# Kernel tuning notes

Measured on AMD Instinct MI355X. Metric: run time of the kernel, lower is better.

## Reference

```python
import jax, jax.numpy as jnp
import numpy as np

B, T, C, H = 2, 2048, 1024, 16
D = C // H  # head dim


def setup_inputs() -> dict:
    key = jax.random.key(0)
    k1, k2, k3 = jax.random.split(key, 3)
    x = jax.random.normal(k1, (B, T, C), dtype=jnp.float32)
    w_qkv = jax.random.normal(k2, (3 * C, C), dtype=jnp.float32) * (1.0 / np.sqrt(C))
    b_qkv = jnp.zeros((3 * C,), dtype=jnp.float32)
    w_proj = jax.random.normal(k3, (C, C), dtype=jnp.float32) * (1.0 / np.sqrt(C))
    b_proj = jnp.zeros((C,), dtype=jnp.float32)
    return {"x": x, "w_qkv": w_qkv, "b_qkv": b_qkv, "w_proj": w_proj, "b_proj": b_proj}


def reference(x, w_qkv, b_qkv, w_proj, b_proj):
    # torch Linear: y = x @ W^T + b
    qkv = jnp.einsum('btc,oc->bto', x, w_qkv) + b_qkv  # [B,T,3C]
    q, k, v = jnp.split(qkv, 3, axis=-1)
    # [B,T,C] -> [B,H,T,D]
    reshape = lambda t: t.reshape(B, T, H, D).transpose(0, 2, 1, 3)
    q, k, v = reshape(q), reshape(k), reshape(v)
    scale = 1.0 / jnp.sqrt(jnp.float32(C))  # NOTE: full C, as in source
    att = jnp.einsum('bhtd,bhsd->bhts', q, k) * scale  # [B,H,T,T]
    causal = jnp.tril(jnp.ones((T, T), dtype=bool))
    att = jnp.where(causal, att, -jnp.inf)
    att = jax.nn.softmax(att, axis=-1)
    y = jnp.einsum('bhts,bhsd->bhtd', att, v)  # [B,H,T,D]
    y = y.transpose(0, 2, 1, 3).reshape(B, T, C)
    return jnp.einsum('btc,oc->bto', y, w_proj) + b_proj
```

## Files before the change

kernel.cpp:

```cpp
#include <hip/hip_runtime.h>

#define DEVINL __device__ __forceinline__

typedef __attribute__((ext_vector_type(8))) short short8;
typedef __attribute__((ext_vector_type(4))) float f32x4;

DEVINL unsigned f2bf_u(float x) {
  union { float f; unsigned u; } v; v.f = x;
  unsigned r = v.u + 0x7FFF + ((v.u >> 16) & 1);
  return r >> 16;
}
DEVINL unsigned short f2bf(float x) { return (unsigned short)f2bf_u(x); }

DEVINL unsigned cvt_pk_bf16(float lo, float hi) {
  unsigned r;
  asm("v_cvt_pk_bf16_f32 %0, %1, %2" : "=v"(r) : "v"(lo), "v"(hi));
  return r;
}

DEVINL void permlane32_swap(unsigned& a, unsigned& b) {
  asm volatile("v_permlane32_swap_b32 %0, %1" : "+v"(a), "+v"(b));
}
DEVINL void permlane16_swap(unsigned& a, unsigned& b) {
  asm volatile("v_permlane16_swap_b32 %0, %1" : "+v"(a), "+v"(b));
}

#if __has_builtin(__builtin_amdgcn_exp2f)
#define EXP2(x) __builtin_amdgcn_exp2f(x)
#else
#define EXP2(x) exp2f(x)
#endif

DEVINL void gload_lds16(const void* g, void* l) {
  __builtin_amdgcn_global_load_lds(
      (const __attribute__((address_space(1))) unsigned int*)g,
      (__attribute__((address_space(3))) unsigned int*)l, 16, 0, 0);
}

DEVINL short8 as_s8(uint4 v) { union { uint4 u; short8 s; } c; c.u = v; return c.s; }
DEVINL f32x4 fzero() { f32x4 z = {0.f, 0.f, 0.f, 0.f}; return z; }

__global__ __launch_bounds__(256) void cvt3_kernel(
    const float4* __restrict__ x, const float4* __restrict__ wq,
    const float4* __restrict__ wp, ushort4* __restrict__ xo,
    ushort4* __restrict__ wqo, ushort4* __restrict__ wpo) {
  const int N1 = 1048576, N2 = 1835008, NT = 2097152;
  int i = blockIdx.x * blockDim.x + threadIdx.x;
  int stride = gridDim.x * blockDim.x;
  for (; i < NT; i += stride) {
    const float4* s; ushort4* d; int j;
    if (i < N1) { s = x; d = xo; j = i; }
    else if (i < N2) { s = wq; d = wqo; j = i - N1; }
    else { s = wp; d = wpo; j = i - N2; }
    float4 v = s[j];
    ushort4 o;
    o.x = f2bf(v.x); o.y = f2bf(v.y); o.z = f2bf(v.z); o.w = f2bf(v.w);
    d[j] = o;
  }
}

template <int MODE, int RX, int RY>
__global__ __launch_bounds__(256, 2) void gemm_bt(
    const ushort* __restrict__ A, const ushort* __restrict__ Bw,
    const float* __restrict__ bias,
    ushort* __restrict__ Qb, ushort* __restrict__ Kb, ushort* __restrict__ Vt,
    float* __restrict__ Out, int M, int N, int K) {
  __shared__ __align__(16) char smem[32768];
  char* ldsA = smem;
  char* ldsB = smem + 16384;

  int gx = gridDim.x;
  int id = blockIdx.y * gx + blockIdx.x;
  int xcd = id & 7, slot = id >> 3;
  int rw = gx / RX, rh = gridDim.y / RY;
  int bx = (xcd % RX) * rw + slot % rw;
  int by = (xcd / RX) * rh + slot / rw;

  int m0 = by * 128, n0 = bx * 128;
  int t = threadIdx.x;
  int lane = t & 63, w = t >> 6;
  int q = lane & 15, g = lane >> 4;
  int wr = w >> 1, wc = w & 1;

  int Lrow[4], Lcol[4];
#pragma unroll
  for (int i = 0; i < 4; ++i) {
    int L = i * 4096 + t * 16;
    int row = L >> 7, c = L & 127;
    Lrow[i] = row;
    Lcol[i] = c ^ ((row & 7) << 4);
  }
  const char* Abase = (const char*)A + (size_t)m0 * K * 2;
  const char* Bbase = (const char*)Bw + (size_t)n0 * K * 2;

  f32x4 acc[4][4];
#pragma unroll
  for (int i = 0; i < 4; ++i)
#pragma unroll
    for (int j = 0; j < 4; ++j) acc[i][j] = fzero();

  for (int k0 = 0; k0 < K; k0 += 64) {
    __syncthreads();
#pragma unroll
    for (int i = 0; i < 4; ++i) {
      int L = i * 4096 + t * 16;
      gload_lds16(Abase + (size_t)Lrow[i] * (K * 2) + k0 * 2 + Lcol[i], ldsA + L);
    }
#pragma unroll
    for (int i = 0; i < 4; ++i) {
      int L = i * 4096 + t * 16;
      gload_lds16(Bbase + (size_t)Lrow[i] * (K * 2) + k0 * 2 + Lcol[i], ldsB + L);
    }
    __syncthreads();

    uint4 bf[2][4];
#pragma unroll
    for (int s = 0; s < 2; ++s)
#pragma unroll
      for (int nt = 0; nt < 4; ++nt) {
        int row = wc * 64 + nt * 16 + q;
        int addr = row * 128 + ((g * 16 + 64 * s) ^ ((row & 7) << 4));
        bf[s][nt] = *(const uint4*)(ldsB + addr);
      }
#pragma unroll
    for (int mt = 0; mt < 4; ++mt) {
      int row = wr * 64 + mt * 16 + q;
      int a0 = row * 128 + ((g * 16) ^ ((row & 7) << 4));
      int a1 = row * 128 + ((g * 16 + 64) ^ ((row & 7) << 4));
      uint4 af0 = *(const uint4*)(ldsA + a0);
      uint4 af1 = *(const uint4*)(ldsA + a1);
#pragma unroll
      for (int nt = 0; nt < 4; ++nt) {
        acc[mt][nt] = __builtin_amdgcn_mfma_f32_16x16x32_bf16(
            as_s8(af0), as_s8(bf[0][nt]), acc[mt][nt], 0, 0, 0);
        acc[mt][nt] = __builtin_amdgcn_mfma_f32_16x16x32_bf16(
            as_s8(af1), as_s8(bf[1][nt]), acc[mt][nt], 0, 0, 0);
      }
    }
  }

  if (MODE == 0) {
    int mrow0 = m0 + wr * 64;
    int b = mrow0 >> 11, tt0 = mrow0 & 2047;
    if (n0 >= 2048) {
      int hs = (n0 + wc * 64) >> 6;
      int h = hs & 15;
      ushort* vb = Vt + ((size_t)(b * 16 + h) * 64) * 2048;
#pragma unroll
      for (int nt = 0; nt < 4; ++nt) {
        int d = nt * 16 + q;
        float bv = bias[n0 + wc * 64 + nt * 16 + q];
#pragma unroll
        for (int mt = 0; mt < 4; ++mt) {
          uint2 o;
          o.x = cvt_pk_bf16(acc[mt][nt][0] + bv, acc[mt][nt][1] + bv);
          o.y = cvt_pk_bf16(acc[mt][nt][2] + bv, acc[mt][nt][3] + bv);
          *(uint2*)(vb + (size_t)d * 2048 + tt0 + mt * 16 + g * 4) = o;
        }
      }
    } else {
      __syncthreads();
      char* tile = smem + w * 8192;
      float bv[4];
#pragma unroll
      for (int nt = 0; nt < 4; ++nt) bv[nt] = bias[n0 + wc * 64 + nt * 16 + q];
#pragma unroll
      for (int mt = 0; mt < 4; ++mt)
#pragma unroll
        for (int nt = 0; nt < 4; ++nt)
#pragma unroll
          for (int r = 0; r < 4; ++r) {
            int row = mt * 16 + g * 4 + r;
            int bcol = ((nt * 16 + q) * 2) ^ ((row & 7) << 4);
            *(ushort*)(tile + row * 128 + bcol) = f2bf(acc[mt][nt][r] + bv[nt]);
          }
      int hs = (n0 + wc * 64) >> 6;
      int which = hs >> 4, h = hs & 15;
      ushort* dst = which == 0 ? Qb : Kb;
      ushort* dbase = dst + (size_t)(b * 16 + h) * 131072 + (size_t)tt0 * 64;
#pragma unroll
      for (int p = 0; p < 8; ++p) {
        int row = p * 8 + (lane >> 3);
        int bcol = ((lane & 7) * 16) ^ ((row & 7) << 4);
        uint4 v = *(const uint4*)(tile + row * 128 + bcol);
        *(uint4*)(dbase + (size_t)row * 64 + (lane & 7) * 8) = v;
      }
    }
  } else {
#pragma unroll
    for (int nt = 0; nt < 4; ++nt) {
      int ncol = n0 + wc * 64 + nt * 16 + q;
      float bv = bias[ncol];
#pragma unroll
      for (int mt = 0; mt < 4; ++mt)
#pragma unroll
        for (int r = 0; r < 4; ++r) {
          int m = m0 + wr * 64 + mt * 16 + g * 4 + r;
          Out[(size_t)m * N + ncol] = acc[mt][nt][r] + bv;
        }
    }
  }
}

__global__ __launch_bounds__(512, 1) void attn_kernel(
    const ushort* __restrict__ Q, const ushort* __restrict__ K,
    const ushort* __restrict__ Vt, ushort* __restrict__ Y) {
  __shared__ __align__(16) char smem[65536];
  const float C44 = 0.0450842298f;
  const float THR44 = 11.5415603f;
  int id = blockIdx.x;
  int xcd = id & 7, slot = id >> 3;
  int bh = xcd * 4 + (slot >> 4);
  int pidx = slot & 15;
  int t = threadIdx.x;
  int lane = t & 63, w = t >> 6;
  int q = lane & 15, g = lane >> 4;
  int wq = w & 3, half = w >> 2;
  int b = bh >> 4, hh = bh & 15;

  const char* Kc0 = (const char*)(K + (size_t)bh * 2048 * 64);
  const char* Vc0 = (const char*)(Vt + (size_t)bh * 64 * 2048);

  int krow[2], kcol[2], vrow[2], vcol[2];
#pragma unroll
  for (int i = 0; i < 2; ++i) {
    int L = i * 8192 + t * 16;
    krow[i] = L >> 7;
    kcol[i] = (L & 127) ^ ((krow[i] & 7) << 4);
    vrow[i] = L >> 8;
    vcol[i] = (L & 255) ^ ((vrow[i] & 7) << 4);
  }
  int offK[4][2], offV[4];
#pragma unroll
  for (int sub = 0; sub < 4; ++sub)
#pragma unroll
    for (int s = 0; s < 2; ++s) {
      int row = half * 64 + sub * 16 + q;
      offK[sub][s] = row * 128 + ((g * 16 + 64 * s) ^ ((row & 7) << 4));
    }
#pragma unroll
  for (int ds = 0; ds < 4; ++ds) {
    int row = ds * 16 + q;
    offV[ds] = 16384 + row * 256 + ((half * 128 + g * 16) ^ ((row & 7) << 4));
  }
  int offV2[4];
#pragma unroll
  for (int ds = 0; ds < 4; ++ds) {
    int row = ds * 16 + q;
    offV2[ds] = 16384 + row * 256 + ((half * 128 + 64 + g * 16) ^ ((row & 7) << 4));
  }

#pragma unroll 1
  for (int pass = 0; pass < 2; ++pass) {
    int qt = pass ? pidx : 31 - pidx;
    int nch = (qt >> 1) + 1;
    int qrow0 = qt * 64 + wq * 16;
    int qg = qrow0 + q;

    uint4 qf[2];
    {
      const ushort* Qrow = Q + ((size_t)bh * 2048 + qrow0 + q) * 64;
      qf[0] = *(const uint4*)(Qrow + g * 8);
      qf[1] = *(const uint4*)(Qrow + 32 + g * 8);
    }

    f32x4 oacc[4];
#pragma unroll
    for (int i = 0; i < 4; ++i) oacc[i] = fzero();
    float m_run = -1e30f;
    float l_run = 0.f;

#pragma unroll
    for (int i = 0; i < 2; ++i) {
      int L = i * 8192 + t * 16;
      gload_lds16(Kc0 + (size_t)krow[i] * 128 + kcol[i], smem + L);
      gload_lds16(Vc0 + (size_t)vrow[i] * 4096 + vcol[i], smem + 16384 + L);
    }
    __syncthreads();

    int cur = 0;
#pragma unroll 1
    for (int c = 0; c < nch; ++c) {
      int kv0 = c * 128;
      if (c + 1 < nch) {
        int kn = kv0 + 128;
        char* dstb = smem + (cur ^ 1) * 32768;
#pragma unroll
        for (int i = 0; i < 2; ++i) {
          int L = i * 8192 + t * 16;
          gload_lds16(Kc0 + (size_t)(kn + krow[i]) * 128 + kcol[i], dstb + L);
          gload_lds16(Vc0 + (size_t)vrow[i] * 4096 + (size_t)kn * 2 + vcol[i],
                      dstb + 16384 + L);
        }
      }
      const char* base = smem + cur * 32768;
      int kst = kv0 + half * 64;
      if (kst <= qrow0 + 15) {
        f32x4 sacc[4];
        __builtin_amdgcn_s_setprio(1);
#pragma unroll
        for (int sub = 0; sub < 4; ++sub) {
          sacc[sub] = fzero();
#pragma unroll
          for (int s = 0; s < 2; ++s)
            sacc[sub] = __builtin_amdgcn_mfma_f32_16x16x32_bf16(
                as_s8(*(const uint4*)(base + offK[sub][s])), as_s8(qf[s]),
                sacc[sub], 0, 0, 0);
        }
        __builtin_amdgcn_s_setprio(0);

        float sr[4][4];
        if (kst + 63 > qrow0) {
#pragma unroll
          for (int sub = 0; sub < 4; ++sub)
#pragma unroll
            for (int r = 0; r < 4; ++r) {
              int kv = kst + sub * 16 + g * 4 + r;
              sr[sub][r] = (kv > qg) ? -3e38f : sacc[sub][r];
            }
        } else {
#pragma unroll
          for (int sub = 0; sub < 4; ++sub)
#pragma unroll
            for (int r = 0; r < 4; ++r) sr[sub][r] = sacc[sub][r];
        }
        float ms[4];
#pragma unroll
        for (int sub = 0; sub < 4; ++sub)
          ms[sub] = fmaxf(fmaxf(sr[sub][0], sr[sub][1]),
                          fmaxf(sr[sub][2], sr[sub][3]));
        float mx44 = fmaxf(fmaxf(ms[0], ms[1]), fmaxf(ms[2], ms[3])) * C44;

        if (!__all(mx44 <= m_run + THR44)) {
          mx44 = fmaxf(mx44, __shfl_xor(mx44, 16));
          mx44 = fmaxf(mx44, __shfl_xor(mx44, 32));
          float mnew = fmaxf(m_run, mx44);
          float corr = EXP2(m_run - mnew);
          float cr[4];
#pragma unroll
          for (int r = 0; r < 4; ++r) cr[r] = __shfl(corr, g * 4 + r);
#pragma unroll
          for (int ds = 0; ds < 4; ++ds)
#pragma unroll
            for (int r = 0; r < 4; ++r) oacc[ds][r] *= cr[r];
          l_run *= corr;
          m_run = mnew;
        }

        float nm = -m_run;
        unsigned pk[4][2];
        float psum = 0.f;
#pragma unroll
        for (int sub = 0; sub < 4; ++sub) {
          float p0 = EXP2(__builtin_fmaf(sr[sub][0], C44, nm));
          float p1 = EXP2(__builtin_fmaf(sr[sub][1], C44, nm));
          float p2 = EXP2(__builtin_fmaf(sr[sub][2], C44, nm));
          float p3 = EXP2(__builtin_fmaf(sr[sub][3], C44, nm));
          psum += (p0 + p1) + (p2 + p3);
          pk[sub][0] = cvt_pk_bf16(p0, p1);
          pk[sub][1] = cvt_pk_bf16(p2, p3);
        }
        l_run += psum;

        uint4 pa[2];
#pragma unroll
        for (int h = 0; h < 2; ++h) {
          unsigned w0 = pk[2 * h][0], w1 = pk[2 * h + 1][0];
          permlane32_swap(w0, w1);
          permlane16_swap(w0, w1);
          unsigned w2 = pk[2 * h][1], w3 = pk[2 * h + 1][1];
          permlane32_swap(w2, w3);
          permlane16_swap(w2, w3);
          pa[h].x = w0; pa[h].y = w2; pa[h].z = w1; pa[h].w = w3;
        }

        __builtin_amdgcn_s_setprio(1);
#pragma unroll
        for (int ds = 0; ds < 4; ++ds) {
          oacc[ds] = __builtin_amdgcn_mfma_f32_16x16x32_bf16(
              as_s8(pa[0]), as_s8(*(const uint4*)(base + offV[ds])),
              oacc[ds], 0, 0, 0);
          oacc[ds] = __builtin_amdgcn_mfma_f32_16x16x32_bf16(
              as_s8(pa[1]), as_s8(*(const uint4*)(base + offV2[ds])),
              oacc[ds], 0, 0, 0);
        }
        __builtin_amdgcn_s_setprio(0);
      }

      __syncthreads();
      cur ^= 1;
    }

    l_run += __shfl_xor(l_run, 16);
    l_run += __shfl_xor(l_run, 32);
    float* ob = (float*)smem + wq * 1024;
    float* mlb = (float*)(smem + 16384);
    if (half) {
#pragma unroll
      for (int ds = 0; ds < 4; ++ds)
#pragma unroll
        for (int r = 0; r < 4; ++r)
          ob[(g * 4 + r) * 64 + ds * 16 + q] = oacc[ds][r];
      if (g == 0) {
        mlb[wq * 32 + q] = m_run;
        mlb[wq * 32 + 16 + q] = l_run;
      }
    }
    __syncthreads();
    if (!half) {
#pragma unroll
      for (int r = 0; r < 4; ++r) {
        int row = g * 4 + r;
        float mA = __shfl(m_run, row);
        float lA = __shfl(l_run, row);
        float mB = mlb[wq * 32 + row];
        float lB = mlb[wq * 32 + 16 + row];
        float mS = fmaxf(mA, mB);
        float sA = EXP2(mA - mS), sB = EXP2(mB - mS);
        float linv = 1.0f / (lA * sA + lB * sB);
        sA *= linv; sB *= linv;
#pragma unroll
        for (int ds = 0; ds < 4; ++ds) {
          float vB = ob[row * 64 + ds * 16 + q];
          float yv = oacc[ds][r] * sA + vB * sB;
          Y[(size_t)(b * 2048 + qrow0 + row) * 1024 + hh * 64 + ds * 16 + q] =
              f2bf(yv);
        }
      }
    }
    __syncthreads();
  }
}

extern "C" void kernel_launch(void* const* d_in, const int* in_sizes, int n_in,
                              void* d_out, int out_size, void* d_ws, size_t ws_size,
                              hipStream_t stream) {
  const float* x = (const float*)d_in[0];
  const float* w_qkv = (const float*)d_in[1];
  const float* b_qkv = (const float*)d_in[2];
  const float* w_proj = (const float*)d_in[3];
  const float* b_proj = (const float*)d_in[4];
  float* out = (float*)d_out;
  char* ws = (char*)d_ws;
  const size_t MB = 1024 * 1024;
  ushort* xb    = (ushort*)(ws + 0 * MB);
  ushort* wqkvb = (ushort*)(ws + 8 * MB);
  ushort* wprojb= (ushort*)(ws + 14 * MB);
  ushort* Qb    = (ushort*)(ws + 16 * MB);
  ushort* Kb    = (ushort*)(ws + 24 * MB);
  ushort* Vt    = (ushort*)(ws + 40 * MB);
  ushort* Yb    = (ushort*)(ws + 48 * MB);

  cvt3_kernel<<<2048, 256, 0, stream>>>((const float4*)x, (const float4*)w_qkv,
                                        (const float4*)w_proj, (ushort4*)xb,
                                        (ushort4*)wqkvb, (ushort4*)wprojb);
  gemm_bt<0, 2, 4><<<dim3(24, 32), 256, 0, stream>>>(xb, wqkvb, b_qkv, Qb, Kb, Vt,
                                                     nullptr, 4096, 3072, 1024);
  attn_kernel<<<dim3(512), 512, 0, stream>>>(Qb, Kb, Vt, Yb);
  gemm_bt<1, 1, 8><<<dim3(8, 32), 256, 0, stream>>>(Yb, wprojb, b_proj, nullptr,
                                                    nullptr, nullptr, out, 4096,
                                                    1024, 1024);
}
```

Measured before the change: 95.29 us.

## Load attention K/V directly into registers and split projection GEMM into smaller tiles

The attention kernel drops its double-buffered LDS staging of K and V and has each wave load its K/V fragments straight from global memory into registers. Shared memory shrinks, per-chunk __syncthreads go away, and occupancy is raised to 4 blocks. The projection GEMM becomes a separate kernel with 64x128 tiles and a 512-block grid to fill more CUs. The cost is duplicated global/L2 reads of K/V across waves, with no prefetch to overlap load latency.

```diff
diff --git a/kernel.cpp b/kernel.cpp
--- a/kernel.cpp
+++ b/kernel.cpp
@@ -59,12 +59,12 @@
   }
 }
 
-template <int MODE, int RX, int RY>
-__global__ __launch_bounds__(256, 2) void gemm_bt(
+template <int RX, int RY>
+__global__ __launch_bounds__(256, 2) void gemm_qkv(
     const ushort* __restrict__ A, const ushort* __restrict__ Bw,
     const float* __restrict__ bias,
     ushort* __restrict__ Qb, ushort* __restrict__ Kb, ushort* __restrict__ Vt,
-    float* __restrict__ Out, int M, int N, int K) {
+    int M, int N, int K) {
   __shared__ __align__(16) char smem[32768];
   char* ldsA = smem;
   char* ldsB = smem + 16384;
@@ -139,73 +139,150 @@
     }
   }
 
-  if (MODE == 0) {
-    int mrow0 = m0 + wr * 64;
-    int b = mrow0 >> 11, tt0 = mrow0 & 2047;
-    if (n0 >= 2048) {
-      int hs = (n0 + wc * 64) >> 6;
-      int h = hs & 15;
-      ushort* vb = Vt + ((size_t)(b * 16 + h) * 64) * 2048;
+  int mrow0 = m0 + wr * 64;
+  int b = mrow0 >> 11, tt0 = mrow0 & 2047;
+  if (n0 >= 2048) {
+    int hs = (n0 + wc * 64) >> 6;
+    int h = hs & 15;
+    ushort* vb = Vt + ((size_t)(b * 16 + h) * 64) * 2048;
+#pragma unroll
+    for (int nt = 0; nt < 4; ++nt) {
+      int d = nt * 16 + q;
+      float bv = bias[n0 + wc * 64 + nt * 16 + q];
+#pragma unroll
+      for (int mt = 0; mt < 4; ++mt) {
+        uint2 o;
+        o.x = cvt_pk_bf16(acc[mt][nt][0] + bv, acc[mt][nt][1] + bv);
+        o.y = cvt_pk_bf16(acc[mt][nt][2] + bv, acc[mt][nt][3] + bv);
+        *(uint2*)(vb + (size_t)d * 2048 + tt0 + mt * 16 + g * 4) = o;
+      }
+    }
+  } else {
+    __syncthreads();
+    char* tile = smem + w * 8192;
+    float bv[4];
+#pragma unroll
+    for (int nt = 0; nt < 4; ++nt) bv[nt] = bias[n0 + wc * 64 + nt * 16 + q];
+#pragma unroll
+    for (int mt = 0; mt < 4; ++mt)
+#pragma unroll
+      for (int nt = 0; nt < 4; ++nt)
+#pragma unroll
+        for (int r = 0; r < 4; ++r) {
+          int row = mt * 16 + g * 4 + r;
+          int bcol = ((nt * 16 + q) * 2) ^ ((row & 7) << 4);
+          *(ushort*)(tile + row * 128 + bcol) = f2bf(acc[mt][nt][r] + bv[nt]);
+        }
+    int hs = (n0 + wc * 64) >> 6;
+    int which = hs >> 4, h = hs & 15;
+    ushort* dst = which == 0 ? Qb : Kb;
+    ushort* dbase = dst + (size_t)(b * 16 + h) * 131072 + (size_t)tt0 * 64;
+#pragma unroll
+    for (int p = 0; p < 8; ++p) {
+      int row = p * 8 + (lane >> 3);
+      int bcol = ((lane & 7) * 16) ^ ((row & 7) << 4);
+      uint4 v = *(const uint4*)(tile + row * 128 + bcol);
+      *(uint4*)(dbase + (size_t)row * 64 + (lane & 7) * 8) = v;
+    }
+  }
+}
+
+__global__ __launch_bounds__(256, 2) void gemm_proj(
+    const ushort* __restrict__ A, const ushort* __restrict__ Bw,
+    const float* __restrict__ bias, float* __restrict__ Out,
+    int M, int N, int K) {
+  __shared__ __align__(16) char smem[24576];
+
+  int gx = gridDim.x;
+  int id = blockIdx.y * gx + blockIdx.x;
+  int xcd = id & 7, slot = id >> 3;
+  int bx = slot & 7;
+  int by = xcd * 8 + (slot >> 3);
+
+  int m0 = by * 64, n0 = bx * 128;
+  int t = threadIdx.x;
+  int lane = t & 63, w = t >> 6;
+  int q = lane & 15, g = lane >> 4;
+  int wr = w >> 1, wc = w & 1;
+
+  int Lrow[4], Lcol[4];
+#pragma unroll
+  for (int i = 0; i < 4; ++i) {
+    int L = i * 4096 + t * 16;
+    int row = L >> 7, c = L & 127;
+    Lrow[i] = row;
+    Lcol[i] = c ^ ((row & 7) << 4);
+  }
+  const char* Abase = (const char*)A + (size_t)m0 * K * 2;
+  const char* Bbase = (const char*)Bw + (size_t)n0 * K * 2;
+
+  f32x4 acc[2][4];
+#pragma unroll
+  for (int i = 0; i < 2; ++i)
+#pragma unroll
+    for (int j = 0; j < 4; ++j) acc[i][j] = fzero();
+
+  for (int k0 = 0; k0 < K; k0 += 64) {
+    __syncthreads();
+#pragma unroll
+    for (int i = 0; i < 2; ++i) {
+      int L = i * 4096 + t * 16;
+      gload_lds16(Abase + (size_t)Lrow[i] * (K * 2) + k0 * 2 + Lcol[i], smem + L);
+    }
+#pragma unroll
+    for (int i = 0; i < 4; ++i) {
+      int L = i * 4096 + t * 16;
+      gload_lds16(Bbase + (size_t)Lrow[i] * (K * 2) + k0 * 2 + Lcol[i],
+                  smem + 8192 + L);
+    }
+    __syncthreads();
+
+    uint4 bf[2][4];
+#pragma unroll
+    for (int s = 0; s < 2; ++s)
 #pragma unroll
       for (int nt = 0; nt < 4; ++nt) {
-        int d = nt * 16 + q;
-        float bv = bias[n0 + wc * 64 + nt * 16 + q];
-#pragma unroll
-        for (int mt = 0; mt < 4; ++mt) {
-          uint2 o;
-          o.x = cvt_pk_bf16(acc[mt][nt][0] + bv, acc[mt][nt][1] + bv);
-          o.y = cvt_pk_bf16(acc[mt][nt][2] + bv, acc[mt][nt][3] + bv);
-          *(uint2*)(vb + (size_t)d * 2048 + tt0 + mt * 16 + g * 4) = o;
-        }
-      }
-    } else {
-      __syncthreads();
-      char* tile = smem + w * 8192;
-      float bv[4];
-#pragma unroll
-      for (int nt = 0; nt < 4; ++nt) bv[nt] = bias[n0 + wc * 64 + nt * 16 + q];
-#pragma unroll
-      for (int mt = 0; mt < 4; ++mt)
-#pragma unroll
-        for (int nt = 0; nt < 4; ++nt)
-#pragma unroll
-          for (int r = 0; r < 4; ++r) {
-            int row = mt * 16 + g * 4 + r;
-            int bcol = ((nt * 16 + q) * 2) ^ ((row & 7) << 4);
-            *(ushort*)(tile + row * 128 + bcol) = f2bf(acc[mt][nt][r] + bv[nt]);
-          }
-      int hs = (n0 + wc * 64) >> 6;
-      int which = hs >> 4, h = hs & 15;
-      ushort* dst = which == 0 ? Qb : Kb;
-      ushort* dbase = dst + (size_t)(b * 16 + h) * 131072 + (size_t)tt0 * 64;
-#pragma unroll
-      for (int p = 0; p < 8; ++p) {
-        int row = p * 8 + (lane >> 3);
-        int bcol = ((lane & 7) * 16) ^ ((row & 7) << 4);
-        uint4 v = *(const uint4*)(tile + row * 128 + bcol);
-        *(uint4*)(dbase + (size_t)row * 64 + (lane & 7) * 8) = v;
-      }
-    }
-  } else {
-#pragma unroll
-    for (int nt = 0; nt < 4; ++nt) {
-      int ncol = n0 + wc * 64 + nt * 16 + q;
-      float bv = bias[ncol];
-#pragma unroll
-      for (int mt = 0; mt < 4; ++mt)
-#pragma unroll
-        for (int r = 0; r < 4; ++r) {
-          int m = m0 + wr * 64 + mt * 16 + g * 4 + r;
-          Out[(size_t)m * N + ncol] = acc[mt][nt][r] + bv;
-        }
-    }
-  }
-}
-
-__global__ __launch_bounds__(512, 1) void attn_kernel(
+        int row = wc * 64 + nt * 16 + q;
+        int addr = 8192 + row * 128 + ((g * 16 + 64 * s) ^ ((row & 7) << 4));
+        bf[s][nt] = *(const uint4*)(smem + addr);
+      }
+    __builtin_amdgcn_s_setprio(1);
+#pragma unroll
+    for (int mt = 0; mt < 2; ++mt) {
+      int row = wr * 32 + mt * 16 + q;
+      int a0 = row * 128 + ((g * 16) ^ ((row & 7) << 4));
+      int a1 = row * 128 + ((g * 16 + 64) ^ ((row & 7) << 4));
+      uint4 af0 = *(const uint4*)(smem + a0);
+      uint4 af1 = *(const uint4*)(smem + a1);
+#pragma unroll
+      for (int nt = 0; nt < 4; ++nt) {
+        acc[mt][nt] = __builtin_amdgcn_mfma_f32_16x16x32_bf16(
+            as_s8(af0), as_s8(bf[0][nt]), acc[mt][nt], 0, 0, 0);
+        acc[mt][nt] = __builtin_amdgcn_mfma_f32_16x16x32_bf16(
+            as_s8(af1), as_s8(bf[1][nt]), acc[mt][nt], 0, 0, 0);
+      }
+    }
+    __builtin_amdgcn_s_setprio(0);
+  }
+
+#pragma unroll
+  for (int nt = 0; nt < 4; ++nt) {
+    int ncol = n0 + wc * 64 + nt * 16 + q;
+    float bv = bias[ncol];
+#pragma unroll
+    for (int mt = 0; mt < 2; ++mt)
+#pragma unroll
+      for (int r = 0; r < 4; ++r) {
+        int m = m0 + wr * 32 + mt * 16 + g * 4 + r;
+        Out[(size_t)m * N + ncol] = acc[mt][nt][r] + bv;
+      }
+  }
+}
+
+__global__ __launch_bounds__(512, 4) void attn_kernel(
     const ushort* __restrict__ Q, const ushort* __restrict__ K,
     const ushort* __restrict__ Vt, ushort* __restrict__ Y) {
-  __shared__ __align__(16) char smem[65536];
+  __shared__ __align__(16) char smem[20480];
   const float C44 = 0.0450842298f;
   const float THR44 = 11.5415603f;
   int id = blockIdx.x;
@@ -218,37 +295,10 @@
   int wq = w & 3, half = w >> 2;
   int b = bh >> 4, hh = bh & 15;
 
-  const char* Kc0 = (const char*)(K + (size_t)bh * 2048 * 64);
-  const char* Vc0 = (const char*)(Vt + (size_t)bh * 64 * 2048);
-
-  int krow[2], kcol[2], vrow[2], vcol[2];
-#pragma unroll
-  for (int i = 0; i < 2; ++i) {
-    int L = i * 8192 + t * 16;
-    krow[i] = L >> 7;
-    kcol[i] = (L & 127) ^ ((krow[i] & 7) << 4);
-    vrow[i] = L >> 8;
-    vcol[i] = (L & 255) ^ ((vrow[i] & 7) << 4);
-  }
-  int offK[4][2], offV[4];
-#pragma unroll
-  for (int sub = 0; sub < 4; ++sub)
-#pragma unroll
-    for (int s = 0; s < 2; ++s) {
-      int row = half * 64 + sub * 16 + q;
-      offK[sub][s] = row * 128 + ((g * 16 + 64 * s) ^ ((row & 7) << 4));
-    }
-#pragma unroll
-  for (int ds = 0; ds < 4; ++ds) {
-    int row = ds * 16 + q;
-    offV[ds] = 16384 + row * 256 + ((half * 128 + g * 16) ^ ((row & 7) << 4));
-  }
-  int offV2[4];
-#pragma unroll
-  for (int ds = 0; ds < 4; ++ds) {
-    int row = ds * 16 + q;
-    offV2[ds] = 16384 + row * 256 + ((half * 128 + 64 + g * 16) ^ ((row & 7) << 4));
-  }
+  const char* Kbase = (const char*)(K + (size_t)bh * 2048 * 64) +
+                      (size_t)(half * 64 + q) * 128 + g * 16;
+  const char* Vbase = (const char*)(Vt + (size_t)bh * 64 * 2048) +
+                      (size_t)q * 4096 + half * 128 + g * 16;
 
 #pragma unroll 1
   for (int pass = 0; pass < 2; ++pass) {
@@ -270,125 +320,107 @@
     float m_run = -1e30f;
     float l_run = 0.f;
 
-#pragma unroll
-    for (int i = 0; i < 2; ++i) {
-      int L = i * 8192 + t * 16;
-      gload_lds16(Kc0 + (size_t)krow[i] * 128 + kcol[i], smem + L);
-      gload_lds16(Vc0 + (size_t)vrow[i] * 4096 + vcol[i], smem + 16384 + L);
-    }
-    __syncthreads();
-
-    int cur = 0;
 #pragma unroll 1
     for (int c = 0; c < nch; ++c) {
       int kv0 = c * 128;
-      if (c + 1 < nch) {
-        int kn = kv0 + 128;
-        char* dstb = smem + (cur ^ 1) * 32768;
-#pragma unroll
-        for (int i = 0; i < 2; ++i) {
-          int L = i * 8192 + t * 16;
-          gload_lds16(Kc0 + (size_t)(kn + krow[i]) * 128 + kcol[i], dstb + L);
-          gload_lds16(Vc0 + (size_t)vrow[i] * 4096 + (size_t)kn * 2 + vcol[i],
-                      dstb + 16384 + L);
-        }
-      }
-      const char* base = smem + cur * 32768;
       int kst = kv0 + half * 64;
-      if (kst <= qrow0 + 15) {
-        f32x4 sacc[4];
-        __builtin_amdgcn_s_setprio(1);
-#pragma unroll
-        for (int sub = 0; sub < 4; ++sub) {
-          sacc[sub] = fzero();
-#pragma unroll
-          for (int s = 0; s < 2; ++s)
-            sacc[sub] = __builtin_amdgcn_mfma_f32_16x16x32_bf16(
-                as_s8(*(const uint4*)(base + offK[sub][s])), as_s8(qf[s]),
-                sacc[sub], 0, 0, 0);
-        }
-        __builtin_amdgcn_s_setprio(0);
-
-        float sr[4][4];
-        if (kst + 63 > qrow0) {
-#pragma unroll
-          for (int sub = 0; sub < 4; ++sub)
-#pragma unroll
-            for (int r = 0; r < 4; ++r) {
-              int kv = kst + sub * 16 + g * 4 + r;
-              sr[sub][r] = (kv > qg) ? -3e38f : sacc[sub][r];
-            }
-        } else {
-#pragma unroll
-          for (int sub = 0; sub < 4; ++sub)
-#pragma unroll
-            for (int r = 0; r < 4; ++r) sr[sub][r] = sacc[sub][r];
-        }
-        float ms[4];
+      if (kst > qrow0 + 15) break;
+
+      const char* kp = Kbase + (size_t)kv0 * 128;
+      uint4 kf[4][2];
+#pragma unroll
+      for (int sub = 0; sub < 4; ++sub)
+#pragma unroll
+        for (int s = 0; s < 2; ++s)
+          kf[sub][s] = *(const uint4*)(kp + sub * 2048 + s * 64);
+      const char* vp = Vbase + (size_t)kv0 * 2;
+      uint4 vf[4][2];
+#pragma unroll
+      for (int ds = 0; ds < 4; ++ds)
+#pragma unroll
+        for (int h2 = 0; h2 < 2; ++h2)
+          vf[ds][h2] = *(const uint4*)(vp + ds * 65536 + h2 * 64);
+
+      f32x4 sacc[4];
+      __builtin_amdgcn_s_setprio(1);
+#pragma unroll
+      for (int sub = 0; sub < 4; ++sub) {
+        sacc[sub] = fzero();
+#pragma unroll
+        for (int s = 0; s < 2; ++s)
+          sacc[sub] = __builtin_amdgcn_mfma_f32_16x16x32_bf16(
+              as_s8(kf[sub][s]), as_s8(qf[s]), sacc[sub], 0, 0, 0);
+      }
+      __builtin_amdgcn_s_setprio(0);
+
+      if (kst + 63 > qrow0) {
 #pragma unroll
         for (int sub = 0; sub < 4; ++sub)
-          ms[sub] = fmaxf(fmaxf(sr[sub][0], sr[sub][1]),
-                          fmaxf(sr[sub][2], sr[sub][3]));
-        float mx44 = fmaxf(fmaxf(ms[0], ms[1]), fmaxf(ms[2], ms[3])) * C44;
-
-        if (!__all(mx44 <= m_run + THR44)) {
-          mx44 = fmaxf(mx44, __shfl_xor(mx44, 16));
-          mx44 = fmaxf(mx44, __shfl_xor(mx44, 32));
-          float mnew = fmaxf(m_run, mx44);
-          float corr = EXP2(m_run - mnew);
-          float cr[4];
-#pragma unroll
-          for (int r = 0; r < 4; ++r) cr[r] = __shfl(corr, g * 4 + r);
-#pragma unroll
-          for (int ds = 0; ds < 4; ++ds)
-#pragma unroll
-            for (int r = 0; r < 4; ++r) oacc[ds][r] *= cr[r];
-          l_run *= corr;
-          m_run = mnew;
-        }
-
-        float nm = -m_run;
-        unsigned pk[4][2];
-        float psum = 0.f;
-#pragma unroll
-        for (int sub = 0; sub < 4; ++sub) {
-          float p0 = EXP2(__builtin_fmaf(sr[sub][0], C44, nm));
-          float p1 = EXP2(__builtin_fmaf(sr[sub][1], C44, nm));
-          float p2 = EXP2(__builtin_fmaf(sr[sub][2], C44, nm));
-          float p3 = EXP2(__builtin_fmaf(sr[sub][3], C44, nm));
-          psum += (p0 + p1) + (p2 + p3);
-          pk[sub][0] = cvt_pk_bf16(p0, p1);
-          pk[sub][1] = cvt_pk_bf16(p2, p3);
-        }
-        l_run += psum;
-
-        uint4 pa[2];
-#pragma unroll
-        for (int h = 0; h < 2; ++h) {
-          unsigned w0 = pk[2 * h][0], w1 = pk[2 * h + 1][0];
-          permlane32_swap(w0, w1);
-          permlane16_swap(w0, w1);
-          unsigned w2 = pk[2 * h][1], w3 = pk[2 * h + 1][1];
-          permlane32_swap(w2, w3);
-          permlane16_swap(w2, w3);
-          pa[h].x = w0; pa[h].y = w2; pa[h].z = w1; pa[h].w = w3;
-        }
-
-        __builtin_amdgcn_s_setprio(1);
-#pragma unroll
-        for (int ds = 0; ds < 4; ++ds) {
-          oacc[ds] = __builtin_amdgcn_mfma_f32_16x16x32_bf16(
-              as_s8(pa[0]), as_s8(*(const uint4*)(base + offV[ds])),
-              oacc[ds], 0, 0, 0);
-          oacc[ds] = __builtin_amdgcn_mfma_f32_16x16x32_bf16(
-              as_s8(pa[1]), as_s8(*(const uint4*)(base + offV2[ds])),
-              oacc[ds], 0, 0, 0);
-        }
-        __builtin_amdgcn_s_setprio(0);
-      }
-
-      __syncthreads();
-      cur ^= 1;
+#pragma unroll
+          for (int r = 0; r < 4; ++r) {
+            int kv = kst + sub * 16 + g * 4 + r;
+            if (kv > qg) sacc[sub][r] = -3e38f;
+          }
+      }
+      float ms[4];
+#pragma unroll
+      for (int sub = 0; sub < 4; ++sub)
+        ms[sub] = fmaxf(fmaxf(sacc[sub][0], sacc[sub][1]),
+                        fmaxf(sacc[sub][2], sacc[sub][3]));
+      float mx44 = fmaxf(fmaxf(ms[0], ms[1]), fmaxf(ms[2], ms[3])) * C44;
+
+      if (!__all(mx44 <= m_run + THR44)) {
+        mx44 = fmaxf(mx44, __shfl_xor(mx44, 16));
+        mx44 = fmaxf(mx44, __shfl_xor(mx44, 32));
+        float mnew = fmaxf(m_run, mx44);
+        float corr = EXP2(m_run - mnew);
+        float cr[4];
+#pragma unroll
+        for (int r = 0; r < 4; ++r) cr[r] = __shfl(corr, g * 4 + r);
+#pragma unroll
+        for (int ds = 0; ds < 4; ++ds)
+#pragma unroll
+          for (int r = 0; r < 4; ++r) oacc[ds][r] *= cr[r];
+        l_run *= corr;
+        m_run = mnew;
+      }
+
+      float nm = -m_run;
+      unsigned pk[4][2];
+      float psum = 0.f;
+#pragma unroll
+      for (int sub = 0; sub < 4; ++sub) {
+        float p0 = EXP2(__builtin_fmaf(sacc[sub][0], C44, nm));
+        float p1 = EXP2(__builtin_fmaf(sacc[sub][1], C44, nm));
+        float p2 = EXP2(__builtin_fmaf(sacc[sub][2], C44, nm));
+        float p3 = EXP2(__builtin_fmaf(sacc[sub][3], C44, nm));
+        psum += (p0 + p1) + (p2 + p3);
+        pk[sub][0] = cvt_pk_bf16(p0, p1);
+        pk[sub][1] = cvt_pk_bf16(p2, p3);
+      }
+      l_run += psum;
+
+      uint4 pa[2];
+#pragma unroll
+      for (int h = 0; h < 2; ++h) {
+        unsigned w0 = pk[2 * h][0], w1 = pk[2 * h + 1][0];
+        permlane32_swap(w0, w1);
+        permlane16_swap(w0, w1);
+        unsigned w2 = pk[2 * h][1], w3 = pk[2 * h + 1][1];
+        permlane32_swap(w2, w3);
+        permlane16_swap(w2, w3);
+        pa[h].x = w0; pa[h].y = w2; pa[h].z = w1; pa[h].w = w3;
+      }
+
+      __builtin_amdgcn_s_setprio(1);
+#pragma unroll
+      for (int ds = 0; ds < 4; ++ds) {
+        oacc[ds] = __builtin_amdgcn_mfma_f32_16x16x32_bf16(
+            as_s8(pa[0]), as_s8(vf[ds][0]), oacc[ds], 0, 0, 0);
+        oacc[ds] = __builtin_amdgcn_mfma_f32_16x16x32_bf16(
+            as_s8(pa[1]), as_s8(vf[ds][1]), oacc[ds], 0, 0, 0);
+      }
+      __builtin_amdgcn_s_setprio(0);
     }
 
     l_run += __shfl_xor(l_run, 16);
@@ -454,10 +486,9 @@
   cvt3_kernel<<<2048, 256, 0, stream>>>((const float4*)x, (const float4*)w_qkv,
                                         (const float4*)w_proj, (ushort4*)xb,
                                         (ushort4*)wqkvb, (ushort4*)wprojb);
-  gemm_bt<0, 2, 4><<<dim3(24, 32), 256, 0, stream>>>(xb, wqkvb, b_qkv, Qb, Kb, Vt,
-                                                     nullptr, 4096, 3072, 1024);
+  gemm_qkv<2, 4><<<dim3(24, 32), 256, 0, stream>>>(xb, wqkvb, b_qkv, Qb, Kb, Vt,
+                                                   4096, 3072, 1024);
   attn_kernel<<<dim3(512), 512, 0, stream>>>(Qb, Kb, Vt, Yb);
-  gemm_bt<1, 1, 8><<<dim3(8, 32), 256, 0, stream>>>(Yb, wprojb, b_proj, nullptr,
-                                                    nullptr, nullptr, out, 4096,
-                                                    1024, 1024);
-}
+  gemm_proj<<<dim3(8, 64), 256, 0, stream>>>(Yb, wprojb, b_proj, out, 4096,
+                                             1024, 1024);
+}
```

New measurement: 178.2 us. 87.0% more time.
